# Kernel tuning notes

Hardware: AMD Instinct MI355X
Metric: run time of the kernel (lower is better)

## Reference

```python
import jax, jax.numpy as jnp
import numpy as np

LAMBDA_C = 0.003
CLAMP_MIN = 1e-12
CLAMP_MAX = 1e12


def setup_inputs() -> dict:
    key = jax.random.key(0)
    k1, k2, k3 = jax.random.split(key, 3)
    B, D, C = 4096, 512, 10000
    embeddings = jax.random.normal(k1, (B, D), dtype=jnp.float32)
    labels = jax.random.randint(k2, (B,), 0, C, dtype=jnp.int64)
    centers = jax.random.normal(k3, (C, D), dtype=jnp.float32)  # nn.Parameter(torch.randn(C, D))
    return {"embeddings": embeddings, "labels": labels, "centers": centers}


def reference(embeddings, labels, centers):
    # Original builds a [B, C] distance matrix, masks to the true-label column,
    # clamps every entry to [1e-12, 1e12], sums, and divides by B.
    # Equivalent efficient form: gather centers[labels], per-row squared L2
    # distance (expanded as ||e||^2 + ||c||^2 - 2 e.c, matching the addmm math),
    # plus the constant B*(C-1)*1e-12 contributed by the clamped masked-out zeros.
    B = embeddings.shape[0]
    C = centers.shape[0]
    c_sel = centers[labels]                                  # [B, D]
    dist = (jnp.sum(embeddings * embeddings, axis=1)
            + jnp.sum(c_sel * c_sel, axis=1)
            - 2.0 * jnp.sum(embeddings * c_sel, axis=1))     # [B]
    dist = jnp.clip(dist, CLAMP_MIN, CLAMP_MAX)
    masked_floor = jnp.float32(B * (C - 1)) * jnp.float32(CLAMP_MIN)
    loss = (jnp.sum(dist) + masked_floor) / B
    return LAMBDA_C * loss
```

## Files before the change

### kernel.cpp

```cpp
#include <hip/hip_runtime.h>


#define LAMBDA_C  0.003f
#define CLAMP_MIN 1e-12f
#define CLAMP_MAX 1e12f

static constexpr int B = 4096;
static constexpr int D = 512;
static constexpr int C = 10000;

__global__ __launch_bounds__(256) void center_loss_kernel(
    const float* __restrict__ emb,
    const int*   __restrict__ labels,
    const float* __restrict__ centers,
    float*       __restrict__ out)
{
    const int wave = threadIdx.x >> 6;
    const int lane = threadIdx.x & 63;
    const int row  = (blockIdx.x << 2) + wave;

    const int label = labels[row];
    const float4* e4 = (const float4*)(emb     + (size_t)row   * D);
    const float4* c4 = (const float4*)(centers + (size_t)label * D);

    float s = 0.0f;
#pragma unroll
    for (int k = 0; k < 2; ++k) {
        const float4 e = e4[lane + (k << 6)];
        const float4 c = c4[lane + (k << 6)];
        const float dx = e.x - c.x;
        const float dy = e.y - c.y;
        const float dz = e.z - c.z;
        const float dw = e.w - c.w;
        s += dx * dx + dy * dy + dz * dz + dw * dw;
    }

#pragma unroll
    for (int off = 32; off > 0; off >>= 1)
        s += __shfl_down(s, off, 64);

    __shared__ float rowsum[4];
    if (lane == 0)
        rowsum[wave] = fminf(fmaxf(s, CLAMP_MIN), CLAMP_MAX);
    __syncthreads();

    if (threadIdx.x == 0) {
        float t = rowsum[0] + rowsum[1] + rowsum[2] + rowsum[3];
        float v = LAMBDA_C * (t / (float)B);
        if (blockIdx.x == 0) {
            v += LAMBDA_C * (((float)B * (float)(C - 1) * CLAMP_MIN) / (float)B);
        }
        atomicAdd(out, v);
    }
}

extern "C" void kernel_launch(void* const* d_in, const int* in_sizes, int n_in,
                              void* d_out, int out_size, void* d_ws, size_t ws_size,
                              hipStream_t stream)
{
    const float* emb     = (const float*)d_in[0];
    const int*   labels  = (const int*)  d_in[1];
    const float* centers = (const float*)d_in[2];
    float*       out     = (float*)d_out;

    hipMemsetAsync(out, 0, sizeof(float), stream);
    center_loss_kernel<<<B / 4, 256, 0, stream>>>(emb, labels, centers, out);
}
```

Baseline: 84.06 us.

## Replace memset and per-block atomics with cooperative grid sync reduction

Drops the hipMemsetAsync and the 1024 per-block float atomics on one address. Each block now writes its partial sum to workspace, the grid synchronizes cooperatively, and block 0 reduces the 1024 partials and writes the result directly. This removes the extra memset launch and atomic contention. In exchange it pays for a grid-wide barrier and needs all 1024 blocks to be co-resident for the cooperative launch.

```diff
diff --git a/kernel.cpp b/kernel.cpp
--- a/kernel.cpp
+++ b/kernel.cpp
@@ -1,4 +1,7 @@
 #include <hip/hip_runtime.h>
+#include <hip/hip_cooperative_groups.h>
+
+namespace cg = cooperative_groups;
 
 
 #define LAMBDA_C  0.003f
@@ -8,11 +11,13 @@
 static constexpr int B = 4096;
 static constexpr int D = 512;
 static constexpr int C = 10000;
+static constexpr int NBLK = B / 4;
 
-__global__ __launch_bounds__(256) void center_loss_kernel(
+__global__ __launch_bounds__(256) void center_loss_coop(
     const float* __restrict__ emb,
     const int*   __restrict__ labels,
     const float* __restrict__ centers,
+    float*       __restrict__ ws,
     float*       __restrict__ out)
 {
     const int wave = threadIdx.x >> 6;
@@ -44,13 +49,27 @@
         rowsum[wave] = fminf(fmaxf(s, CLAMP_MIN), CLAMP_MAX);
     __syncthreads();
 
-    if (threadIdx.x == 0) {
-        float t = rowsum[0] + rowsum[1] + rowsum[2] + rowsum[3];
-        float v = LAMBDA_C * (t / (float)B);
-        if (blockIdx.x == 0) {
-            v += LAMBDA_C * (((float)B * (float)(C - 1) * CLAMP_MIN) / (float)B);
+    if (threadIdx.x == 0)
+        ws[blockIdx.x] = rowsum[0] + rowsum[1] + rowsum[2] + rowsum[3];
+
+    cg::this_grid().sync();
+
+    if (blockIdx.x == 0) {
+        const float4 v = ((const float4*)ws)[threadIdx.x];
+        float t = v.x + v.y + v.z + v.w;
+#pragma unroll
+        for (int off = 32; off > 0; off >>= 1)
+            t += __shfl_down(t, off, 64);
+
+        __shared__ float wsum[4];
+        if (lane == 0) wsum[wave] = t;
+        __syncthreads();
+
+        if (threadIdx.x == 0) {
+            const float total = wsum[0] + wsum[1] + wsum[2] + wsum[3];
+            const float masked_floor = (float)B * (float)(C - 1) * CLAMP_MIN;
+            out[0] = LAMBDA_C * ((total + masked_floor) / (float)B);
         }
-        atomicAdd(out, v);
     }
 }
 
@@ -61,8 +80,11 @@
     const float* emb     = (const float*)d_in[0];
     const int*   labels  = (const int*)  d_in[1];
     const float* centers = (const float*)d_in[2];
+    float*       ws      = (float*)d_ws;
     float*       out     = (float*)d_out;
 
-    hipMemsetAsync(out, 0, sizeof(float), stream);
-    center_loss_kernel<<<B / 4, 256, 0, stream>>>(emb, labels, centers, out);
+    void* args[] = { (void*)&emb, (void*)&labels, (void*)&centers,
+                     (void*)&ws, (void*)&out };
+    hipLaunchCooperativeKernel((const void*)center_loss_coop,
+                               dim3(NBLK), dim3(256), args, 0, stream);
 }
```

After: 150.0 us. 78.4% more time.
